# Performance work log

Measured on AMD Instinct MI355X. Metric: run time of the kernel, lower is better.

The kernel has to match this reference:

```python
import jax, jax.numpy as jnp
import numpy as np

SCALE = 4


def _dist_mats():
    # Replicates matrix_generation() with scale=4 (numpy constants).
    s = SCALE
    x = np.array([-2.0, -1.0, 1.0, 2.0], np.float32)  # arange(-2,3) with the 0 removed
    base = np.broadcast_to(x[None, :], (s, s)).copy()  # varies along width
    dm = np.stack([base, base.T])[None]                # [1,2,4,4]
    xr = np.broadcast_to(np.arange(1, s + 1, dtype=np.float32)[None, :], (s, s)).copy()
    xc = xr.T
    dm1 = dm.copy(); dm1[:, 0] = s - xr + 1
    dm2 = dm.copy(); dm2[:, 0] = xr
    dm3 = dm.copy(); dm3[:, 1] = s - xc + 1
    dm4 = dm.copy(); dm4[:, 1] = xc
    # NOTE: forward() reuses dm1..dm4 for the 4 diagonal directions (as in the
    # original code, which indexes self.distance_matrix1..4 for matrices 5..8).
    return dm, dm1, dm2, dm3, dm4


def _mlp(x, w0, w1, w2, w3):
    # 1x1-conv stack 66->32->16->8->1, no bias, LeakyReLU(0.01) between.
    h = jax.nn.leaky_relu(jnp.einsum('bchw,oc->bohw', x, w0))
    h = jax.nn.leaky_relu(jnp.einsum('bchw,oc->bohw', h, w1))
    h = jax.nn.leaky_relu(jnp.einsum('bchw,oc->bohw', h, w2))
    return jnp.einsum('bchw,oc->bohw', h, w3)


def setup_inputs() -> dict:
    key = jax.random.key(0)
    ks = jax.random.split(key, 8)
    B, C, H, W = 2, 32, 256, 512
    lr_feature = jax.random.normal(ks[0], (B, C, H // SCALE, W // SCALE), jnp.float32)
    hr_feature = jax.random.normal(ks[1], (B, C, H, W), jnp.float32)
    lr_feature_r = jax.random.normal(ks[2], (B, C, H // SCALE, W // SCALE), jnp.float32)
    hr_feature_r = jax.random.normal(ks[3], (B, C, H, W), jnp.float32)
    # kaiming_normal_(mode='fan_out') for 1x1 conv: std = sqrt(2 / out_ch)
    def kaiming(k, shape):
        return jax.random.normal(k, shape, jnp.float32) * np.sqrt(2.0 / shape[0]).astype(np.float32)
    w0 = kaiming(ks[4], (32, 66))
    w1 = kaiming(ks[5], (16, 32))
    w2 = kaiming(ks[6], (8, 16))
    w3 = kaiming(ks[7], (1, 8))
    return {'lr_feature': lr_feature, 'hr_feature': hr_feature,
            'lr_feature_r': lr_feature_r, 'hr_feature_r': hr_feature_r,
            'w0': w0, 'w1': w1, 'w2': w2, 'w3': w3}


def reference(lr_feature, hr_feature, lr_feature_r, hr_feature_r, w0, w1, w2, w3):
    s = SCALE
    B, _, H, W = hr_feature.shape
    dm, dm1, dm2, dm3, dm4 = _dist_mats()
    tile = lambda d: jnp.tile(jnp.asarray(d), (B, 1, H // s, W // s))  # [B,2,H,W]
    D, D1, D2, D3, D4 = tile(dm), tile(dm1), tile(dm2), tile(dm3), tile(dm4)
    # nearest-neighbor upsample of lr feature by scale in both spatial dims
    lr = jnp.repeat(jnp.repeat(lr_feature, s, axis=3), s, axis=2)
    hr = hr_feature
    pad1 = jnp.full((B, 1, H, s), -100.0, hr.dtype)  # width padding
    pad2 = jnp.full((B, 1, s, W), -100.0, hr.dtype)  # height padding
    cat = lambda *xs: jnp.concatenate(xs, axis=1)
    m = lambda x: _mlp(x, w0, w1, w2, w3)

    w_c = m(cat(lr, hr, D))
    w_l = jnp.concatenate([pad1, m(cat(lr[:, :, :, :-s], hr[:, :, :, s:], D1[:, :, :, :-s]))], -1)
    w_r = jnp.concatenate([m(cat(lr[:, :, :, s:], hr[:, :, :, :-s], D2[:, :, :, s:])), pad1], -1)
    w_t = jnp.concatenate([pad2, m(cat(lr[:, :, :-s, :], hr[:, :, s:, :], D3[:, :, :-s, :]))], -2)
    w_b = jnp.concatenate([m(cat(lr[:, :, s:, :], hr[:, :, :-s, :], D4[:, :, s:, :])), pad2], -2)
    w_lt = jnp.concatenate([pad2, jnp.concatenate(
        [pad1[:, :, s:, :], m(cat(lr[:, :, :-s, :-s], hr[:, :, s:, s:], D1[:, :, :-s, :-s]))], -1)], -2)
    w_rt = jnp.concatenate([pad2, jnp.concatenate(
        [m(cat(lr[:, :, :-s, s:], hr[:, :, s:, :-s], D2[:, :, :-s, s:])), pad1[:, :, s:, :]], -1)], -2)
    w_lb = jnp.concatenate([jnp.concatenate(
        [pad1[:, :, s:, :], m(cat(lr[:, :, s:, :-s], hr[:, :, :-s, s:], D3[:, :, s:, :-s]))], -1), pad2], -2)
    w_rb = jnp.concatenate([jnp.concatenate(
        [m(cat(lr[:, :, s:, s:], hr[:, :, :-s, :-s], D4[:, :, s:, s:])), pad1[:, :, :-s, :]], -1), pad2], -2)

    weight_all = jnp.concatenate([w_c, w_l, w_r, w_t, w_b, w_lt, w_rt, w_lb, w_rb], axis=1)
    # Original returns the 9 channel slices of softmax(weight_all, dim=1);
    # we return the full normalized [B,9,H,W] tensor (slice i == output i).
    return jax.nn.softmax(weight_all, axis=1)
```

## Files before the change

### kernel.cpp

```cpp
#include <hip/hip_runtime.h>
#include <math.h>

#define SC 4
#define BB 2
#define CC 32
#define HH 256
#define WW 512
#define CH (HH / SC)
#define CW (WW / SC)

using f16x8 = __attribute__((ext_vector_type(8))) _Float16;
using f32x4 = __attribute__((ext_vector_type(4))) float;
using f32x2 = __attribute__((ext_vector_type(2))) float;

constexpr int K_dh[9] = {0, 0, 0, -1, 1, -1, -1, 1, 1};
constexpr int K_dw[9] = {0, -1, 1, 0, 0, -1, 1, -1, 1};
constexpr int K_s0[9] = {0, 1, 2, 0, 0, 1, 2, 0, 0};
constexpr int K_s1[9] = {0, 0, 0, 1, 2, 0, 0, 1, 2};

template <int CTRL>
__device__ __forceinline__ float dpp_add(float v) {
    union { float f; int i; } u, r;
    u.f = v;
    r.i = __builtin_amdgcn_update_dpp(0, u.i, CTRL, 0xF, 0xF, true);
    return v + r.f;
}

__device__ __forceinline__ float sum8(float v) {
    v = dpp_add<0xB1>(v);
    v = dpp_add<0x4E>(v);
    v = dpp_add<0x141>(v);
    return v;
}

__global__ __launch_bounds__(256) void alr_prepass(const float* __restrict__ lr,
                                                   const float* __restrict__ w0,
                                                   float* __restrict__ alr) {
    const int idx = blockIdx.x * 256 + threadIdx.x;
    if (idx >= BB * CH * CW) return;
    const int b = idx / (CH * CW);
    const int cell = idx - b * (CH * CW);
    const float* lp = lr + (size_t)b * CC * CH * CW + cell;
    float lv[32];
#pragma unroll
    for (int c = 0; c < 32; c++) lv[c] = lp[(size_t)c * (CH * CW)];
    float acc[32];
#pragma unroll
    for (int o = 0; o < 32; o++) {
        float a = 0.f;
#pragma unroll
        for (int c = 0; c < 32; c++) a = fmaf(lv[c], w0[o * 66 + c], a);
        acc[o] = a;
    }
    float4* op = (float4*)(alr + (size_t)idx * 32);
#pragma unroll
    for (int j = 0; j < 8; j++)
        op[j] = make_float4(acc[4 * j], acc[4 * j + 1], acc[4 * j + 2], acc[4 * j + 3]);
}

template <bool USE_WS>
__global__ __launch_bounds__(256, 4) void ercm_mfma(const float* __restrict__ hr,
                                                    const float* __restrict__ lr,
                                                    const float* __restrict__ alr,
                                                    const float* __restrict__ w0,
                                                    const float* __restrict__ w1,
                                                    const float* __restrict__ w2,
                                                    const float* __restrict__ w3,
                                                    float* __restrict__ out) {
    __shared__ _Float16 s_alr[30 * 40];
    __shared__ _Float16 s_ahr[4][16 * 40];
    __shared__ _Float16 s_d2[4][16 * 40];

    const int tid = threadIdx.x;
    const int lane = tid & 63;
    const int ty = tid >> 6;
    const int m16 = lane & 15;
    const int q = lane >> 4;
    const int bx = blockIdx.x;
    const int by = blockIdx.y;
    const int b = blockIdx.z;
    const int h = by * 4 + ty;
    const int wp0 = bx * 32;
    const size_t HW = (size_t)HH * WW;

    const int cy0 = by, cx0 = bx * 8;
    if (USE_WS) {
        for (int i = tid; i < 30 * 32; i += 256) {
            const int c = i & 31, cell = i >> 5;
            const int row = cell / 10, col = cell - row * 10;
            const int gcy = cy0 - 1 + row, gcx = cx0 - 1 + col;
            float v = 0.f;
            if ((unsigned)gcy < (unsigned)CH && (unsigned)gcx < (unsigned)CW)
                v = alr[(((size_t)b * CH + gcy) * CW + gcx) * 32 + c];
            s_alr[cell * 40 + c] = (_Float16)v;
        }
    } else {
        for (int i = tid; i < 30 * 32; i += 256) {
            const int o = i & 31, cell = i >> 5;
            const int row = cell / 10, col = cell - row * 10;
            const int gcy = cy0 - 1 + row, gcx = cx0 - 1 + col;
            float a = 0.f;
            if ((unsigned)gcy < (unsigned)CH && (unsigned)gcx < (unsigned)CW) {
                const float* lp = lr + (size_t)b * CC * CH * CW + (size_t)gcy * CW + gcx;
#pragma unroll
                for (int c = 0; c < 32; c++) a = fmaf(lp[(size_t)c * (CH * CW)], w0[o * 66 + c], a);
            }
            s_alr[cell * 40 + o] = (_Float16)a;
        }
    }

    f16x8 w1B, w0hB0, w0hB1, w2B;
    {
        const float* p1 = w1 + m16 * 32 + q * 8;
        const float* p00 = w0 + m16 * 66 + 32 + q * 8;
        const float* p01 = w0 + (m16 + 16) * 66 + 32 + q * 8;
        const bool w2ok = (m16 < 8) && (q < 2);
#pragma unroll
        for (int j = 0; j < 8; j++) {
            w1B[j] = (_Float16)p1[j];
            w0hB0[j] = (_Float16)p00[j];
            w0hB1[j] = (_Float16)p01[j];
            w2B[j] = (_Float16)(w2ok ? w2[m16 * 16 + q * 8 + j] : 0.f);
        }
    }
    f32x2 w0d0v[4], w0d1v[4];
#pragma unroll
    for (int jp = 0; jp < 4; jp++) {
        w0d0v[jp] = f32x2{w0[(q * 8 + 2 * jp) * 66 + 64], w0[(q * 8 + 2 * jp + 1) * 66 + 64]};
        w0d1v[jp] = f32x2{w0[(q * 8 + 2 * jp) * 66 + 65], w0[(q * 8 + 2 * jp + 1) * 66 + 65]};
    }
    const float w3v = (m16 < 8) ? w3[m16] : 0.f;

    const int xm = m16 & 3;
    const float xv = (float)(xm < 2 ? xm - 2 : xm - 1);
    const float x1 = (float)(4 - xm), x2 = (float)(xm + 1);
    const int ym = h & 3;
    const float yv = (float)(ym < 2 ? ym - 2 : ym - 1);
    const float y1 = (float)(4 - ym), y2 = (float)(ym + 1);

    _Float16* sa = s_ahr[ty];
    _Float16* sd = s_d2[ty];
#pragma unroll
    for (int r = 0; r < 4; r++) sd[(q * 4 + r) * 40 + 16 + m16] = (_Float16)0.f;

    __syncthreads();

    const float* hp = hr + (size_t)b * CC * HW + (size_t)h * WW + wp0;

#pragma unroll 1
    for (int t = 0; t < 2; t++) {
        f16x8 a;
#pragma unroll
        for (int j = 0; j < 8; j++) a[j] = (_Float16)hp[(size_t)(q * 8 + j) * HW + t * 16 + m16];
        f32x4 acc0 = {0.f, 0.f, 0.f, 0.f}, acc1 = {0.f, 0.f, 0.f, 0.f};
        acc0 = __builtin_amdgcn_mfma_f32_16x16x32_f16(a, w0hB0, acc0, 0, 0, 0);
        acc1 = __builtin_amdgcn_mfma_f32_16x16x32_f16(a, w0hB1, acc1, 0, 0, 0);
#pragma unroll
        for (int r = 0; r < 4; r++) {
            sa[(q * 4 + r) * 40 + m16] = (_Float16)acc0[r];
            sa[(q * 4 + r) * 40 + 16 + m16] = (_Float16)acc1[r];
        }
        const f16x8 ahv = *(const f16x8*)&sa[m16 * 40 + q * 8];
        f32x2 ah2[4];
#pragma unroll
        for (int jp = 0; jp < 4; jp++)
            ah2[jp] = f32x2{(float)ahv[2 * jp], (float)ahv[2 * jp + 1]};

        const _Float16* alp = &s_alr[((t * 16 + m16) >> 2) * 40 + q * 8];
        const int wown = wp0 + t * 16 + q * 4 + xm;

        float l[9];
#pragma unroll
        for (int d = 0; d < 9; d++) {
            const int dh = K_dh[d], dw = K_dw[d];
            const float d0 = (K_s0[d] == 0) ? xv : ((K_s0[d] == 1) ? x1 : x2);
            const float d1 = (K_s1[d] == 0) ? yv : ((K_s1[d] == 1) ? y1 : y2);
            const f32x2 d0v = {d0, d0}, d1v = {d1, d1};

            const f16x8 alv = *(const f16x8*)(alp + ((1 + dh) * 10 + (1 + dw)) * 40);
            f16x8 a1;
#pragma unroll
            for (int jp = 0; jp < 4; jp++) {
                f32x2 v = ah2[jp] + f32x2{(float)alv[2 * jp], (float)alv[2 * jp + 1]};
                v = __builtin_elementwise_fma(w0d0v[jp], d0v, v);
                v = __builtin_elementwise_fma(w0d1v[jp], d1v, v);
                v = __builtin_elementwise_max(v, v * 0.01f);
                a1[2 * jp] = (_Float16)v[0];
                a1[2 * jp + 1] = (_Float16)v[1];
            }
            f32x4 acc2 = {0.f, 0.f, 0.f, 0.f};
            acc2 = __builtin_amdgcn_mfma_f32_16x16x32_f16(a1, w1B, acc2, 0, 0, 0);
#pragma unroll
            for (int r = 0; r < 4; r++) {
                const float v = fmaxf(acc2[r], 0.01f * acc2[r]);
                sd[(q * 4 + r) * 40 + m16] = (_Float16)v;
            }
            const f16x8 a3 = *(const f16x8*)&sd[m16 * 40 + q * 8];
            f32x4 acc3 = {0.f, 0.f, 0.f, 0.f};
            acc3 = __builtin_amdgcn_mfma_f32_16x16x32_f16(a3, w2B, acc3, 0, 0, 0);

            float sr[4];
#pragma unroll
            for (int r = 0; r < 4; r++)
                sr[r] = sum8(w3v * fmaxf(acc3[r], 0.01f * acc3[r]));
            float lv = sr[0];
            lv = (xm == 1) ? sr[1] : lv;
            lv = (xm == 2) ? sr[2] : lv;
            lv = (xm == 3) ? sr[3] : lv;
            const bool ok = ((unsigned)(h + 4 * dh) < (unsigned)HH) &&
                            ((unsigned)(wown + 4 * dw) < (unsigned)WW);
            l[d] = ok ? lv : -100.0f;
        }

        float mx = l[0];
#pragma unroll
        for (int d = 1; d < 9; d++) mx = fmaxf(mx, l[d]);
        float s = 0.f;
#pragma unroll
        for (int d = 0; d < 9; d++) {
            l[d] = __expf(l[d] - mx);
            s += l[d];
        }
        const float inv = __builtin_amdgcn_rcpf(s);
        if (m16 < 4) {
            float* op = out + (size_t)b * 9 * HW + (size_t)h * WW + (wp0 + t * 16 + q * 4 + m16);
#pragma unroll
            for (int d = 0; d < 9; d++) op[(size_t)d * HW] = l[d] * inv;
        }
    }
}

extern "C" void kernel_launch(void* const* d_in, const int* in_sizes, int n_in,
                              void* d_out, int out_size, void* d_ws, size_t ws_size,
                              hipStream_t stream) {
    const float* lr = (const float*)d_in[0];
    const float* hr = (const float*)d_in[1];
    const float* w0 = (const float*)d_in[4];
    const float* w1 = (const float*)d_in[5];
    const float* w2 = (const float*)d_in[6];
    const float* w3 = (const float*)d_in[7];
    float* out = (float*)d_out;

    const size_t alr_bytes = (size_t)BB * CH * CW * 32 * sizeof(float);
    dim3 grid(WW / 32, HH / 4, BB);

    if (ws_size >= alr_bytes) {
        float* alr = (float*)d_ws;
        alr_prepass<<<(BB * CH * CW + 255) / 256, 256, 0, stream>>>(lr, w0, alr);
        ercm_mfma<true><<<grid, 256, 0, stream>>>(hr, lr, alr, w0, w1, w2, w3, out);
    } else {
        ercm_mfma<false><<<grid, 256, 0, stream>>>(hr, lr, nullptr, w0, w1, w2, w3, out);
    }
}
```

Measured before the change: 153.0 us.

## Transpose MFMA operands, pass layer2 outputs via bpermute, and process both tiles together

The MLP MFMAs now compute the transposed product (weights as A, activations as B), so each lane's accumulator already holds a pixel's channel values. Layer-2 outputs move into layer-3 operands through ds_bpermute instead of an LDS store/load round trip, which removes the s_d2 buffer. The final 8-channel dot uses per-lane partial sums plus a swizzle and a shuffle instead of DPP reductions and lane selection. The two 16-pixel tiles are unrolled and interleaved to give more independent MFMA work, at the cost of higher register pressure.

```diff
diff --git a/kernel.cpp b/kernel.cpp
--- a/kernel.cpp
+++ b/kernel.cpp
@@ -18,19 +18,15 @@
 constexpr int K_s0[9] = {0, 1, 2, 0, 0, 1, 2, 0, 0};
 constexpr int K_s1[9] = {0, 0, 0, 1, 2, 0, 0, 1, 2};
 
-template <int CTRL>
-__device__ __forceinline__ float dpp_add(float v) {
-    union { float f; int i; } u, r;
-    u.f = v;
-    r.i = __builtin_amdgcn_update_dpp(0, u.i, CTRL, 0xF, 0xF, true);
-    return v + r.f;
-}
-
-__device__ __forceinline__ float sum8(float v) {
-    v = dpp_add<0xB1>(v);
-    v = dpp_add<0x4E>(v);
-    v = dpp_add<0x141>(v);
-    return v;
+__device__ __forceinline__ float swz_x16(float v) {
+    return __int_as_float(__builtin_amdgcn_ds_swizzle(__float_as_int(v), 0x401F));
+}
+
+__device__ __forceinline__ int pack2h(float a, float b) {
+    union { _Float16 h[2]; int i; } u;
+    u.h[0] = (_Float16)a;
+    u.h[1] = (_Float16)b;
+    return u.i;
 }
 
 __global__ __launch_bounds__(256) void alr_prepass(const float* __restrict__ lr,
@@ -68,8 +64,7 @@
                                                     const float* __restrict__ w3,
                                                     float* __restrict__ out) {
     __shared__ _Float16 s_alr[30 * 40];
-    __shared__ _Float16 s_ahr[4][16 * 40];
-    __shared__ _Float16 s_d2[4][16 * 40];
+    __shared__ _Float16 s_ahr[4][32 * 40];
 
     const int tid = threadIdx.x;
     const int lane = tid & 63;
@@ -129,7 +124,9 @@
         w0d0v[jp] = f32x2{w0[(q * 8 + 2 * jp) * 66 + 64], w0[(q * 8 + 2 * jp + 1) * 66 + 64]};
         w0d1v[jp] = f32x2{w0[(q * 8 + 2 * jp) * 66 + 65], w0[(q * 8 + 2 * jp + 1) * 66 + 65]};
     }
-    const float w3v = (m16 < 8) ? w3[m16] : 0.f;
+    float w3c[4];
+#pragma unroll
+    for (int r = 0; r < 4; r++) w3c[r] = (q < 2) ? w3[q * 4 + r] : 0.f;
 
     const int xm = m16 & 3;
     const float xv = (float)(xm < 2 ? xm - 2 : xm - 1);
@@ -138,94 +135,172 @@
     const float yv = (float)(ym < 2 ? ym - 2 : ym - 1);
     const float y1 = (float)(4 - ym), y2 = (float)(ym + 1);
 
+    const int A0 = ((m16 + 32 * q) & 63) << 2;
+    const int A1 = ((m16 + 32 * q + 16) & 63) << 2;
+
     _Float16* sa = s_ahr[ty];
-    _Float16* sd = s_d2[ty];
-#pragma unroll
-    for (int r = 0; r < 4; r++) sd[(q * 4 + r) * 40 + 16 + m16] = (_Float16)0.f;
 
     __syncthreads();
 
     const float* hp = hr + (size_t)b * CC * HW + (size_t)h * WW + wp0;
 
-#pragma unroll 1
-    for (int t = 0; t < 2; t++) {
-        f16x8 a;
-#pragma unroll
-        for (int j = 0; j < 8; j++) a[j] = (_Float16)hp[(size_t)(q * 8 + j) * HW + t * 16 + m16];
-        f32x4 acc0 = {0.f, 0.f, 0.f, 0.f}, acc1 = {0.f, 0.f, 0.f, 0.f};
-        acc0 = __builtin_amdgcn_mfma_f32_16x16x32_f16(a, w0hB0, acc0, 0, 0, 0);
-        acc1 = __builtin_amdgcn_mfma_f32_16x16x32_f16(a, w0hB1, acc1, 0, 0, 0);
+    f16x8 aT0, aT1;
+#pragma unroll
+    for (int j = 0; j < 8; j++) {
+        aT0[j] = (_Float16)hp[(size_t)(q * 8 + j) * HW + m16];
+        aT1[j] = (_Float16)hp[(size_t)(q * 8 + j) * HW + 16 + m16];
+    }
+    {
+        f32x4 p00 = {0.f, 0.f, 0.f, 0.f}, p01 = {0.f, 0.f, 0.f, 0.f};
+        f32x4 p10 = {0.f, 0.f, 0.f, 0.f}, p11 = {0.f, 0.f, 0.f, 0.f};
+        p00 = __builtin_amdgcn_mfma_f32_16x16x32_f16(aT0, w0hB0, p00, 0, 0, 0);
+        p01 = __builtin_amdgcn_mfma_f32_16x16x32_f16(aT0, w0hB1, p01, 0, 0, 0);
+        p10 = __builtin_amdgcn_mfma_f32_16x16x32_f16(aT1, w0hB0, p10, 0, 0, 0);
+        p11 = __builtin_amdgcn_mfma_f32_16x16x32_f16(aT1, w0hB1, p11, 0, 0, 0);
 #pragma unroll
         for (int r = 0; r < 4; r++) {
-            sa[(q * 4 + r) * 40 + m16] = (_Float16)acc0[r];
-            sa[(q * 4 + r) * 40 + 16 + m16] = (_Float16)acc1[r];
-        }
-        const f16x8 ahv = *(const f16x8*)&sa[m16 * 40 + q * 8];
-        f32x2 ah2[4];
+            const int row = q * 4 + r;
+            sa[row * 40 + m16] = (_Float16)p00[r];
+            sa[row * 40 + 16 + m16] = (_Float16)p01[r];
+            sa[(16 + row) * 40 + m16] = (_Float16)p10[r];
+            sa[(16 + row) * 40 + 16 + m16] = (_Float16)p11[r];
+        }
+    }
+    const f16x8 ahv0 = *(const f16x8*)&sa[m16 * 40 + q * 8];
+    const f16x8 ahv1 = *(const f16x8*)&sa[(16 + m16) * 40 + q * 8];
+    f32x2 ah0[4], ah1[4];
+#pragma unroll
+    for (int jp = 0; jp < 4; jp++) {
+        ah0[jp] = f32x2{(float)ahv0[2 * jp], (float)ahv0[2 * jp + 1]};
+        ah1[jp] = f32x2{(float)ahv1[2 * jp], (float)ahv1[2 * jp + 1]};
+    }
+
+    const _Float16* alp0 = &s_alr[(m16 >> 2) * 40 + q * 8];
+    const _Float16* alp1 = &s_alr[(4 + (m16 >> 2)) * 40 + q * 8];
+    const int wown0 = wp0 + m16;
+    const int wown1 = wp0 + 16 + m16;
+
+    float l0[9], l1[9];
+#pragma unroll
+    for (int d = 0; d < 9; d++) {
+        const int dh = K_dh[d], dw = K_dw[d];
+        const float d0 = (K_s0[d] == 0) ? xv : ((K_s0[d] == 1) ? x1 : x2);
+        const float d1 = (K_s1[d] == 0) ? yv : ((K_s1[d] == 1) ? y1 : y2);
+        const f32x2 d0v = {d0, d0}, d1v = {d1, d1};
+        const int off = ((1 + dh) * 10 + (1 + dw)) * 40;
+
+        f32x2 dd[4];
 #pragma unroll
         for (int jp = 0; jp < 4; jp++)
-            ah2[jp] = f32x2{(float)ahv[2 * jp], (float)ahv[2 * jp + 1]};
-
-        const _Float16* alp = &s_alr[((t * 16 + m16) >> 2) * 40 + q * 8];
-        const int wown = wp0 + t * 16 + q * 4 + xm;
-
-        float l[9];
+            dd[jp] = __builtin_elementwise_fma(w0d0v[jp], d0v, w0d1v[jp] * d1v);
+
+        const f16x8 alv0 = *(const f16x8*)(alp0 + off);
+        const f16x8 alv1 = *(const f16x8*)(alp1 + off);
+        f16x8 a1_0, a1_1;
+#pragma unroll
+        for (int jp = 0; jp < 4; jp++) {
+            f32x2 v0 = ah0[jp] + f32x2{(float)alv0[2 * jp], (float)alv0[2 * jp + 1]};
+            f32x2 v1 = ah1[jp] + f32x2{(float)alv1[2 * jp], (float)alv1[2 * jp + 1]};
+            v0 = v0 + dd[jp];
+            v1 = v1 + dd[jp];
+            v0 = __builtin_elementwise_max(v0, v0 * 0.01f);
+            v1 = __builtin_elementwise_max(v1, v1 * 0.01f);
+            a1_0[2 * jp] = (_Float16)v0[0];
+            a1_0[2 * jp + 1] = (_Float16)v0[1];
+            a1_1[2 * jp] = (_Float16)v1[0];
+            a1_1[2 * jp + 1] = (_Float16)v1[1];
+        }
+        f32x4 c2_0 = {0.f, 0.f, 0.f, 0.f}, c2_1 = {0.f, 0.f, 0.f, 0.f};
+        c2_0 = __builtin_amdgcn_mfma_f32_16x16x32_f16(w1B, a1_0, c2_0, 0, 0, 0);
+        c2_1 = __builtin_amdgcn_mfma_f32_16x16x32_f16(w1B, a1_1, c2_1, 0, 0, 0);
+
+        f16x8 a3_0, a3_1;
+        {
+            float e0 = fmaxf(c2_0[0], 0.01f * c2_0[0]), e1 = fmaxf(c2_0[1], 0.01f * c2_0[1]);
+            float e2 = fmaxf(c2_0[2], 0.01f * c2_0[2]), e3 = fmaxf(c2_0[3], 0.01f * c2_0[3]);
+            const int pk0 = pack2h(e0, e1), pk1 = pack2h(e2, e3);
+            union { int i[4]; f16x8 v; } u;
+            u.i[0] = __builtin_amdgcn_ds_bpermute(A0, pk0);
+            u.i[1] = __builtin_amdgcn_ds_bpermute(A0, pk1);
+            u.i[2] = __builtin_amdgcn_ds_bpermute(A1, pk0);
+            u.i[3] = __builtin_amdgcn_ds_bpermute(A1, pk1);
+            a3_0 = u.v;
+        }
+        {
+            float e0 = fmaxf(c2_1[0], 0.01f * c2_1[0]), e1 = fmaxf(c2_1[1], 0.01f * c2_1[1]);
+            float e2 = fmaxf(c2_1[2], 0.01f * c2_1[2]), e3 = fmaxf(c2_1[3], 0.01f * c2_1[3]);
+            const int pk0 = pack2h(e0, e1), pk1 = pack2h(e2, e3);
+            union { int i[4]; f16x8 v; } u;
+            u.i[0] = __builtin_amdgcn_ds_bpermute(A0, pk0);
+            u.i[1] = __builtin_amdgcn_ds_bpermute(A0, pk1);
+            u.i[2] = __builtin_amdgcn_ds_bpermute(A1, pk0);
+            u.i[3] = __builtin_amdgcn_ds_bpermute(A1, pk1);
+            a3_1 = u.v;
+        }
+        f32x4 c3_0 = {0.f, 0.f, 0.f, 0.f}, c3_1 = {0.f, 0.f, 0.f, 0.f};
+        c3_0 = __builtin_amdgcn_mfma_f32_16x16x32_f16(w2B, a3_0, c3_0, 0, 0, 0);
+        c3_1 = __builtin_amdgcn_mfma_f32_16x16x32_f16(w2B, a3_1, c3_1, 0, 0, 0);
+
+        {
+            float part = 0.f;
+#pragma unroll
+            for (int r = 0; r < 4; r++) {
+                const float lv = fmaxf(c3_0[r], 0.01f * c3_0[r]);
+                part = fmaf(w3c[r], lv, part);
+            }
+            float s2 = part + swz_x16(part);
+            const float lg = s2 + __shfl_xor(s2, 32, 64);
+            const bool ok = ((unsigned)(h + 4 * dh) < (unsigned)HH) &&
+                            ((unsigned)(wown0 + 4 * dw) < (unsigned)WW);
+            l0[d] = ok ? lg : -100.0f;
+        }
+        {
+            float part = 0.f;
+#pragma unroll
+            for (int r = 0; r < 4; r++) {
+                const float lv = fmaxf(c3_1[r], 0.01f * c3_1[r]);
+                part = fmaf(w3c[r], lv, part);
+            }
+            float s2 = part + swz_x16(part);
+            const float lg = s2 + __shfl_xor(s2, 32, 64);
+            const bool ok = ((unsigned)(h + 4 * dh) < (unsigned)HH) &&
+                            ((unsigned)(wown1 + 4 * dw) < (unsigned)WW);
+            l1[d] = ok ? lg : -100.0f;
+        }
+    }
+
+    {
+        float mx = l0[0];
+#pragma unroll
+        for (int d = 1; d < 9; d++) mx = fmaxf(mx, l0[d]);
+        float s = 0.f;
 #pragma unroll
         for (int d = 0; d < 9; d++) {
-            const int dh = K_dh[d], dw = K_dw[d];
-            const float d0 = (K_s0[d] == 0) ? xv : ((K_s0[d] == 1) ? x1 : x2);
-            const float d1 = (K_s1[d] == 0) ? yv : ((K_s1[d] == 1) ? y1 : y2);
-            const f32x2 d0v = {d0, d0}, d1v = {d1, d1};
-
-            const f16x8 alv = *(const f16x8*)(alp + ((1 + dh) * 10 + (1 + dw)) * 40);
-            f16x8 a1;
-#pragma unroll
-            for (int jp = 0; jp < 4; jp++) {
-                f32x2 v = ah2[jp] + f32x2{(float)alv[2 * jp], (float)alv[2 * jp + 1]};
-                v = __builtin_elementwise_fma(w0d0v[jp], d0v, v);
-                v = __builtin_elementwise_fma(w0d1v[jp], d1v, v);
-                v = __builtin_elementwise_max(v, v * 0.01f);
-                a1[2 * jp] = (_Float16)v[0];
-                a1[2 * jp + 1] = (_Float16)v[1];
-            }
-            f32x4 acc2 = {0.f, 0.f, 0.f, 0.f};
-            acc2 = __builtin_amdgcn_mfma_f32_16x16x32_f16(a1, w1B, acc2, 0, 0, 0);
-#pragma unroll
-            for (int r = 0; r < 4; r++) {
-                const float v = fmaxf(acc2[r], 0.01f * acc2[r]);
-                sd[(q * 4 + r) * 40 + m16] = (_Float16)v;
-            }
-            const f16x8 a3 = *(const f16x8*)&sd[m16 * 40 + q * 8];
-            f32x4 acc3 = {0.f, 0.f, 0.f, 0.f};
-            acc3 = __builtin_amdgcn_mfma_f32_16x16x32_f16(a3, w2B, acc3, 0, 0, 0);
-
-            float sr[4];
-#pragma unroll
-            for (int r = 0; r < 4; r++)
-                sr[r] = sum8(w3v * fmaxf(acc3[r], 0.01f * acc3[r]));
-            float lv = sr[0];
-            lv = (xm == 1) ? sr[1] : lv;
-            lv = (xm == 2) ? sr[2] : lv;
-            lv = (xm == 3) ? sr[3] : lv;
-            const bool ok = ((unsigned)(h + 4 * dh) < (unsigned)HH) &&
-                            ((unsigned)(wown + 4 * dw) < (unsigned)WW);
-            l[d] = ok ? lv : -100.0f;
-        }
-
-        float mx = l[0];
-#pragma unroll
-        for (int d = 1; d < 9; d++) mx = fmaxf(mx, l[d]);
+            l0[d] = __expf(l0[d] - mx);
+            s += l0[d];
+        }
+        const float inv = __builtin_amdgcn_rcpf(s);
+        if (lane < 16) {
+            float* op = out + (size_t)b * 9 * HW + (size_t)h * WW + wown0;
+#pragma unroll
+            for (int d = 0; d < 9; d++) op[(size_t)d * HW] = l0[d] * inv;
+        }
+    }
+    {
+        float mx = l1[0];
+#pragma unroll
+        for (int d = 1; d < 9; d++) mx = fmaxf(mx, l1[d]);
         float s = 0.f;
 #pragma unroll
         for (int d = 0; d < 9; d++) {
-            l[d] = __expf(l[d] - mx);
-            s += l[d];
+            l1[d] = __expf(l1[d] - mx);
+            s += l1[d];
         }
         const float inv = __builtin_amdgcn_rcpf(s);
-        if (m16 < 4) {
-            float* op = out + (size_t)b * 9 * HW + (size_t)h * WW + (wp0 + t * 16 + q * 4 + m16);
-#pragma unroll
-            for (int d = 0; d < 9; d++) op[(size_t)d * HW] = l[d] * inv;
+        if (lane < 16) {
+            float* op = out + (size_t)b * 9 * HW + (size_t)h * WW + wown1;
+#pragma unroll
+            for (int d = 0; d < 9; d++) op[(size_t)d * HW] = l1[d] * inv;
         }
     }
 }
```

Result: faster. 146.4 us (-4.3%).
